# Kernel optimization log

Measured on AMD Instinct MI355X. Metric: run time of the kernel, lower is better.

Reference implementation:

```python
import jax, jax.numpy as jnp
import numpy as np

N = 50000
NEG_SLOPE = 0.2


def add_self_loops(edge_index, n):
    loop = jnp.arange(n, dtype=edge_index.dtype)
    return jnp.concatenate([edge_index, jnp.stack([loop, loop])], axis=1)


def gatv2_conv(x, edge_index, Wl, bl, Wr, br, att, bias):
    """PyG GATv2Conv (share_weights=False, concat=True, add_self_loops applied by caller).
    x: [N, Fin]; edge_index: [2, E] with row0=src(j), row1=dst(i); att: [H, D].
    Returns (out [N, H*D], alpha [E, H])."""
    src, dst = edge_index[0], edge_index[1]
    H, D = att.shape
    n = x.shape[0]
    xl = (x @ Wl + bl).reshape(n, H, D)   # source-side transform
    xr = (x @ Wr + br).reshape(n, H, D)   # target-side transform
    e = jax.nn.leaky_relu(xl[src] + xr[dst], NEG_SLOPE)        # [E, H, D]
    logit = jnp.einsum('ehd,hd->eh', e, att)                    # [E, H]
    # segment softmax over edges grouped by target node
    lmax = jax.ops.segment_max(logit, dst, num_segments=n)      # [N, H]
    ex = jnp.exp(logit - lmax[dst])
    denom = jax.ops.segment_sum(ex, dst, num_segments=n)
    alpha = ex / denom[dst]                                     # [E, H]
    out = jax.ops.segment_sum(alpha[:, :, None] * xl[src], dst, num_segments=n)  # [N, H, D]
    return out.reshape(n, H * D) + bias, alpha


def setup_inputs() -> dict:
    key = jax.random.key(0)
    ks = jax.random.split(key, 16)
    E = 400000
    x = jax.random.normal(ks[0], (N, 23), dtype=jnp.float32)
    edge_index = jax.random.randint(ks[1], (2, E), 0, N, dtype=jnp.int64)
    H1, D1 = 8, 64
    F1 = H1 * D1  # 512
    s = 0.1
    return {
        'x': x,
        'edge_index': edge_index,
        'Wl1': jax.random.normal(ks[2], (23, F1), dtype=jnp.float32) * s,
        'bl1': jnp.zeros((F1,), jnp.float32),
        'Wr1': jax.random.normal(ks[3], (23, F1), dtype=jnp.float32) * s,
        'br1': jnp.zeros((F1,), jnp.float32),
        'att1': jax.random.normal(ks[4], (H1, D1), dtype=jnp.float32) * s,
        'bias1': jnp.zeros((F1,), jnp.float32),
        'Wl2': jax.random.normal(ks[5], (F1, 1), dtype=jnp.float32) * s,
        'bl2': jnp.zeros((1,), jnp.float32),
        'Wr2': jax.random.normal(ks[6], (F1, 1), dtype=jnp.float32) * s,
        'br2': jnp.zeros((1,), jnp.float32),
        'att2': jax.random.normal(ks[7], (1, 1), dtype=jnp.float32) * s,
        'bias2': jnp.zeros((1,), jnp.float32),
    }


def reference(x, edge_index, Wl1, bl1, Wr1, br1, att1, bias1,
              Wl2, bl2, Wr2, br2, att2, bias2):
    ei = add_self_loops(edge_index, N)
    h, _ = gatv2_conv(x, ei, Wl1, bl1, Wr1, br1, att1, bias1)
    h = jax.nn.relu(h)
    h, alpha = gatv2_conv(h, ei, Wl2, bl2, Wr2, br2, att2, bias2)
    return h, alpha
```

## Files before the change

### kernel.cpp

```cpp
#include <hip/hip_runtime.h>
#include <math.h>

#define NN 50000
#define E0 400000
#define EE 450000
#define FF 512
#define G1 2048
#define NPB 25
#define EPB 220
#define WAVES_TOTAL (G1 * 4)
#define MAXD 64
#define LOG2E 1.44269504f

typedef _Float16 h2 __attribute__((ext_vector_type(2)));

__device__ __forceinline__ h2 uas_h2(unsigned u) { union { unsigned u; h2 h; } c; c.u = u; return c.h; }
__device__ __forceinline__ unsigned h2as_u(h2 h) { union { unsigned u; h2 h; } c; c.h = h; return c.u; }
__device__ __forceinline__ unsigned packh(float a, float b) {
    h2 hh = { (_Float16)a, (_Float16)b };
    return h2as_u(hh);
}
__device__ __forceinline__ float leaky(float v) { return fmaxf(v, 0.2f * v); }

__global__ __launch_bounds__(256) void k_predeg(
    const float* __restrict__ x,
    const float* __restrict__ Wl1, const float* __restrict__ bl1,
    const float* __restrict__ Wr1, const float* __restrict__ br1,
    const int* __restrict__ ei,
    unsigned* __restrict__ xlh, unsigned* __restrict__ xrh,
    int* __restrict__ cnt, int* __restrict__ src_sl, int* __restrict__ eid_sl)
{
    __shared__ unsigned sxh[NPB * 12];
    int b = blockIdx.x, t = threadIdx.x;

    {
        int e0 = b * EPB;
        int e1 = e0 + EPB; if (e1 > EE) e1 = EE;
        for (int e = e0 + t; e < e1; e += 256) {
            int src, dst;
            if (e < E0) { src = ei[e]; dst = ei[E0 + e]; }
            else        { src = e - E0; dst = src; }
            int p = atomicAdd(&cnt[dst], 1);
            if (p < MAXD) {
                src_sl[(size_t)dst * MAXD + p] = src;
                eid_sl[(size_t)dst * MAXD + p] = e;
            }
        }
    }

    int i0 = b * NPB;
    int i1 = i0 + NPB; if (i1 > NN) i1 = NN;
    int nnod = i1 - i0;
    for (int k = t; k < nnod * 12; k += 256) {
        int n = k / 12, j = k - n * 12;
        const float* row = x + (size_t)(i0 + n) * 23;
        float f0 = row[2 * j];
        float f1 = (2 * j + 1 < 23) ? row[2 * j + 1] : 0.f;
        sxh[n * 12 + j] = packh(f0, f1);
    }

    int c0 = 2 * t, c1 = 2 * t + 1;
    h2 wl0[12], wl1[12], wr0[12], wr1[12];
#pragma unroll
    for (int j = 0; j < 12; j++) {
        int r0 = 2 * j, r1 = 2 * j + 1;
        float a, b2;
        a = Wl1[r0 * FF + c0]; b2 = (r1 < 23) ? Wl1[r1 * FF + c0] : 0.f;
        wl0[j] = (h2){ (_Float16)a, (_Float16)b2 };
        a = Wl1[r0 * FF + c1]; b2 = (r1 < 23) ? Wl1[r1 * FF + c1] : 0.f;
        wl1[j] = (h2){ (_Float16)a, (_Float16)b2 };
        a = Wr1[r0 * FF + c0]; b2 = (r1 < 23) ? Wr1[r1 * FF + c0] : 0.f;
        wr0[j] = (h2){ (_Float16)a, (_Float16)b2 };
        a = Wr1[r0 * FF + c1]; b2 = (r1 < 23) ? Wr1[r1 * FF + c1] : 0.f;
        wr1[j] = (h2){ (_Float16)a, (_Float16)b2 };
    }
    float bl0 = bl1[c0], bl1s = bl1[c1];
    float br0 = br1[c0], br1s = br1[c1];
    __syncthreads();

    const uint4* S = (const uint4*)sxh;
    for (int n = 0; n < nnod; n++) {
        uint4 xa = S[n * 3 + 0];
        uint4 xb = S[n * 3 + 1];
        uint4 xc = S[n * 3 + 2];
        h2 xv[12] = { uas_h2(xa.x), uas_h2(xa.y), uas_h2(xa.z), uas_h2(xa.w),
                      uas_h2(xb.x), uas_h2(xb.y), uas_h2(xb.z), uas_h2(xb.w),
                      uas_h2(xc.x), uas_h2(xc.y), uas_h2(xc.z), uas_h2(xc.w) };
        float al0 = bl0, al1 = bl1s, ar0 = br0, ar1 = br1s;
#pragma unroll
        for (int j = 0; j < 12; j++) {
            al0 = __builtin_amdgcn_fdot2(wl0[j], xv[j], al0, false);
            al1 = __builtin_amdgcn_fdot2(wl1[j], xv[j], al1, false);
            ar0 = __builtin_amdgcn_fdot2(wr0[j], xv[j], ar0, false);
            ar1 = __builtin_amdgcn_fdot2(wr1[j], xv[j], ar1, false);
        }
        xlh[(size_t)(i0 + n) * 256 + t] = packh(al0, al1);
        xrh[(size_t)(i0 + n) * 256 + t] = packh(ar0, ar1);
    }
}

__global__ __launch_bounds__(256) void k_layer1(
    const uint4* __restrict__ xlh, const uint4* __restrict__ xrh,
    const float* __restrict__ att, const float* __restrict__ bias1,
    const float* __restrict__ Wl2, const float* __restrict__ bl2,
    const float* __restrict__ Wr2, const float* __restrict__ br2,
    const int* __restrict__ cnt, const int* __restrict__ src_sl,
    float* __restrict__ xl2, float* __restrict__ xr2)
{
    int t = threadIdx.x;
    int l = t & 63;
    int wid = blockIdx.x * 4 + (t >> 6);

    float4 atA = ((const float4*)att)[2 * l];
    float4 atB = ((const float4*)att)[2 * l + 1];
    h2 a6_0 = { (_Float16)(0.6f * LOG2E * atA.x), (_Float16)(0.6f * LOG2E * atA.y) };
    h2 a6_1 = { (_Float16)(0.6f * LOG2E * atA.z), (_Float16)(0.6f * LOG2E * atA.w) };
    h2 a6_2 = { (_Float16)(0.6f * LOG2E * atB.x), (_Float16)(0.6f * LOG2E * atB.y) };
    h2 a6_3 = { (_Float16)(0.6f * LOG2E * atB.z), (_Float16)(0.6f * LOG2E * atB.w) };
    h2 a4_0 = { (_Float16)(0.4f * LOG2E * atA.x), (_Float16)(0.4f * LOG2E * atA.y) };
    h2 a4_1 = { (_Float16)(0.4f * LOG2E * atA.z), (_Float16)(0.4f * LOG2E * atA.w) };
    h2 a4_2 = { (_Float16)(0.4f * LOG2E * atB.x), (_Float16)(0.4f * LOG2E * atB.y) };
    h2 a4_3 = { (_Float16)(0.4f * LOG2E * atB.z), (_Float16)(0.4f * LOG2E * atB.w) };
    float bl2v = bl2[0], br2v = br2[0];

    for (int i = wid; i < NN; i += WAVES_TOTAL) {
        uint4 xq = xrh[(size_t)i * 64 + l];
        h2 q0 = uas_h2(xq.x), q1 = uas_h2(xq.y), q2 = uas_h2(xq.z), q3 = uas_h2(xq.w);

        float s = 0.f;
        h2 A0 = { 0, 0 }, A1 = { 0, 0 }, A2 = { 0, 0 }, A3 = { 0, 0 };

        int dg = cnt[i]; if (dg > MAXD) dg = MAXD;
        int myj = (l < dg) ? src_sl[(size_t)i * MAXD + l] : 0;

        int j0 = __builtin_amdgcn_readlane(myj, 0);
        uint4 r0 = xlh[(size_t)j0 * 64 + l];
        uint4 r1 = r0;
        if (dg > 1) r1 = xlh[(size_t)__builtin_amdgcn_readlane(myj, 1) * 64 + l];

        for (int p = 0; p < dg; p++) {
            uint4 rn = r0;
            if (p + 2 < dg)
                rn = xlh[(size_t)__builtin_amdgcn_readlane(myj, p + 2) * 64 + l];

            h2 p0 = uas_h2(r0.x), p1 = uas_h2(r0.y), p2 = uas_h2(r0.z), p3 = uas_h2(r0.w);
            h2 t0 = p0 + q0, t1 = p1 + q1, t2 = p2 + q2, t3 = p3 + q3;
            h2 b0 = uas_h2(h2as_u(t0) & 0x7fff7fffu);
            h2 b1 = uas_h2(h2as_u(t1) & 0x7fff7fffu);
            h2 b2 = uas_h2(h2as_u(t2) & 0x7fff7fffu);
            h2 b3 = uas_h2(h2as_u(t3) & 0x7fff7fffu);
            float part = 0.f;
            part = __builtin_amdgcn_fdot2(a6_0, t0, part, false);
            part = __builtin_amdgcn_fdot2(a4_0, b0, part, false);
            part = __builtin_amdgcn_fdot2(a6_1, t1, part, false);
            part = __builtin_amdgcn_fdot2(a4_1, b1, part, false);
            part = __builtin_amdgcn_fdot2(a6_2, t2, part, false);
            part = __builtin_amdgcn_fdot2(a4_2, b2, part, false);
            part = __builtin_amdgcn_fdot2(a6_3, t3, part, false);
            part = __builtin_amdgcn_fdot2(a4_3, b3, part, false);
            part += __shfl_xor(part, 1, 64);
            part += __shfl_xor(part, 2, 64);
            part += __shfl_xor(part, 4, 64);
            float wv = exp2f(part);
            s += wv;
            _Float16 wh = (_Float16)wv;
            h2 w2 = { wh, wh };
            A0 += w2 * p0;
            A1 += w2 * p1;
            A2 += w2 * p2;
            A3 += w2 * p3;
            r0 = r1; r1 = rn;
        }

        float inv = 1.f / s;
        float4 bA = ((const float4*)bias1)[2 * l];
        float4 bB = ((const float4*)bias1)[2 * l + 1];
        float h0 = fmaxf(fmaf((float)A0[0], inv, bA.x), 0.f);
        float h1 = fmaxf(fmaf((float)A0[1], inv, bA.y), 0.f);
        float h2v = fmaxf(fmaf((float)A1[0], inv, bA.z), 0.f);
        float h3 = fmaxf(fmaf((float)A1[1], inv, bA.w), 0.f);
        float h4 = fmaxf(fmaf((float)A2[0], inv, bB.x), 0.f);
        float h5 = fmaxf(fmaf((float)A2[1], inv, bB.y), 0.f);
        float h6 = fmaxf(fmaf((float)A3[0], inv, bB.z), 0.f);
        float h7 = fmaxf(fmaf((float)A3[1], inv, bB.w), 0.f);

        float4 wlA = ((const float4*)Wl2)[2 * l];
        float4 wlB = ((const float4*)Wl2)[2 * l + 1];
        float4 wrA = ((const float4*)Wr2)[2 * l];
        float4 wrB = ((const float4*)Wr2)[2 * l + 1];
        float pl = h0 * wlA.x + h1 * wlA.y + h2v * wlA.z + h3 * wlA.w
                 + h4 * wlB.x + h5 * wlB.y + h6 * wlB.z + h7 * wlB.w;
        float pr = h0 * wrA.x + h1 * wrA.y + h2v * wrA.z + h3 * wrA.w
                 + h4 * wrB.x + h5 * wrB.y + h6 * wrB.z + h7 * wrB.w;
#pragma unroll
        for (int o = 32; o > 0; o >>= 1) {
            pl += __shfl_xor(pl, o, 64);
            pr += __shfl_xor(pr, o, 64);
        }
        if (l == 0) {
            xl2[i] = pl + bl2v;
            xr2[i] = pr + br2v;
        }
    }
}

__global__ void k_layer2(const float* __restrict__ xl2, const float* __restrict__ xr2,
                         const float* __restrict__ att2, const float* __restrict__ bias2,
                         const int* __restrict__ cnt, const int* __restrict__ src_sl,
                         const int* __restrict__ eid_sl, float* __restrict__ out)
{
    int i = blockIdx.x * blockDim.x + threadIdx.x;
    if (i >= NN) return;
    int dg = cnt[i]; if (dg > MAXD) dg = MAXD;
    const int* sp = src_sl + (size_t)i * MAXD;
    const int* ep = eid_sl + (size_t)i * MAXD;
    float xri = xr2[i];
    float a2l = att2[0] * LOG2E;
    float s = 0.f, num = 0.f;
    for (int p = 0; p < dg; p++) {
        float v = xl2[sp[p]];
        float w = exp2f(leaky(v + xri) * a2l);
        s += w;
        num = fmaf(w, v, num);
    }
    out[i] = num / s + bias2[0];
    float inv = 1.f / s;
    for (int p = 0; p < dg; p++) {
        float v = xl2[sp[p]];
        float w = exp2f(leaky(v + xri) * a2l);
        out[NN + ep[p]] = w * inv;
    }
}

extern "C" void kernel_launch(void* const* d_in, const int* in_sizes, int n_in,
                              void* d_out, int out_size, void* d_ws, size_t ws_size,
                              hipStream_t stream)
{
    const float* x     = (const float*)d_in[0];
    const int*   ei    = (const int*)d_in[1];
    const float* Wl1   = (const float*)d_in[2];
    const float* bl1   = (const float*)d_in[3];
    const float* Wr1   = (const float*)d_in[4];
    const float* br1   = (const float*)d_in[5];
    const float* att1  = (const float*)d_in[6];
    const float* bias1 = (const float*)d_in[7];
    const float* Wl2   = (const float*)d_in[8];
    const float* bl2   = (const float*)d_in[9];
    const float* Wr2   = (const float*)d_in[10];
    const float* br2   = (const float*)d_in[11];
    const float* att2  = (const float*)d_in[12];
    const float* bias2 = (const float*)d_in[13];
    float* out = (float*)d_out;

    char* ws = (char*)d_ws;
    unsigned* xlh  = (unsigned*)ws; ws += (size_t)NN * 256 * 4;
    unsigned* xrh  = (unsigned*)ws; ws += (size_t)NN * 256 * 4;
    float* xl2     = (float*)ws;    ws += (size_t)NN * 4;
    float* xr2     = (float*)ws;    ws += (size_t)NN * 4;
    int* cnt       = (int*)ws;      ws += (size_t)NN * 4;
    int* src_sl    = (int*)ws;      ws += (size_t)NN * MAXD * 4;
    int* eid_sl    = (int*)ws;      ws += (size_t)NN * MAXD * 4;

    hipMemsetAsync(cnt, 0, (size_t)NN * 4, stream);

    k_predeg<<<G1, 256, 0, stream>>>(x, Wl1, bl1, Wr1, br1, ei, xlh, xrh,
                                     cnt, src_sl, eid_sl);
    k_layer1<<<G1, 256, 0, stream>>>((const uint4*)xlh, (const uint4*)xrh,
                                     att1, bias1, Wl2, bl2, Wr2, br2,
                                     cnt, src_sl, xl2, xr2);
    k_layer2<<<(NN + 255) / 256, 256, 0, stream>>>(xl2, xr2, att2, bias2,
                                                   cnt, src_sl, eid_sl, out);
}
```

Measured before the change: 238.7 us.

## Fuse three kernels into one persistent kernel with software grid barriers

Merges the degree/projection, layer-1 aggregation and layer-2 kernels into a single persistent kernel of 1024 blocks. The stages are separated by atomic-counter grid barriers instead of kernel launch boundaries. Per-block work sizes are doubled to match the halved grid, and the barrier counters are zeroed by the existing memset. This removes two launch gaps but adds spin-wait barrier cost. The barriers assume all 1024 blocks are resident at once, which is not guaranteed by a plain launch, and a block that is not resident would deadlock.

Measured after the change: 737.5 us. 3.09x slower.

```diff
diff --git a/kernel.cpp b/kernel.cpp
--- a/kernel.cpp
+++ b/kernel.cpp
@@ -5,10 +5,10 @@
 #define E0 400000
 #define EE 450000
 #define FF 512
-#define G1 2048
-#define NPB 25
-#define EPB 220
-#define WAVES_TOTAL (G1 * 4)
+#define GRID 1024
+#define NPB 49
+#define EPB 440
+#define L1W (GRID * 4)
 #define MAXD 64
 #define LOG2E 1.44269504f
 
@@ -22,13 +22,32 @@
 }
 __device__ __forceinline__ float leaky(float v) { return fmaxf(v, 0.2f * v); }
 
-__global__ __launch_bounds__(256) void k_predeg(
-    const float* __restrict__ x,
+__device__ __forceinline__ void gridbar(int* bar, int* rel, int t)
+{
+    __threadfence();
+    __syncthreads();
+    if (t == 0) {
+        int v = atomicAdd(bar, 1);
+        if (v == GRID - 1) atomicExch(rel, 1);
+        else while (atomicAdd(rel, 0) == 0) __builtin_amdgcn_s_sleep(16);
+    }
+    __syncthreads();
+    __threadfence();
+}
+
+__global__ __launch_bounds__(256, 4) void k_mega(
+    const float* __restrict__ x, const int* __restrict__ ei,
     const float* __restrict__ Wl1, const float* __restrict__ bl1,
     const float* __restrict__ Wr1, const float* __restrict__ br1,
-    const int* __restrict__ ei,
+    const float* __restrict__ att1, const float* __restrict__ bias1,
+    const float* __restrict__ Wl2, const float* __restrict__ bl2,
+    const float* __restrict__ Wr2, const float* __restrict__ br2,
+    const float* __restrict__ att2, const float* __restrict__ bias2,
+    float* __restrict__ out,
     unsigned* __restrict__ xlh, unsigned* __restrict__ xrh,
-    int* __restrict__ cnt, int* __restrict__ src_sl, int* __restrict__ eid_sl)
+    float* __restrict__ xl2, float* __restrict__ xr2,
+    int* __restrict__ cnt, int* __restrict__ bar,
+    int* __restrict__ src_sl, int* __restrict__ eid_sl)
 {
     __shared__ unsigned sxh[NPB * 12];
     int b = blockIdx.x, t = threadIdx.x;
@@ -46,189 +65,182 @@
                 eid_sl[(size_t)dst * MAXD + p] = e;
             }
         }
-    }
-
-    int i0 = b * NPB;
-    int i1 = i0 + NPB; if (i1 > NN) i1 = NN;
-    int nnod = i1 - i0;
-    for (int k = t; k < nnod * 12; k += 256) {
-        int n = k / 12, j = k - n * 12;
-        const float* row = x + (size_t)(i0 + n) * 23;
-        float f0 = row[2 * j];
-        float f1 = (2 * j + 1 < 23) ? row[2 * j + 1] : 0.f;
-        sxh[n * 12 + j] = packh(f0, f1);
-    }
-
-    int c0 = 2 * t, c1 = 2 * t + 1;
-    h2 wl0[12], wl1[12], wr0[12], wr1[12];
-#pragma unroll
-    for (int j = 0; j < 12; j++) {
-        int r0 = 2 * j, r1 = 2 * j + 1;
-        float a, b2;
-        a = Wl1[r0 * FF + c0]; b2 = (r1 < 23) ? Wl1[r1 * FF + c0] : 0.f;
-        wl0[j] = (h2){ (_Float16)a, (_Float16)b2 };
-        a = Wl1[r0 * FF + c1]; b2 = (r1 < 23) ? Wl1[r1 * FF + c1] : 0.f;
-        wl1[j] = (h2){ (_Float16)a, (_Float16)b2 };
-        a = Wr1[r0 * FF + c0]; b2 = (r1 < 23) ? Wr1[r1 * FF + c0] : 0.f;
-        wr0[j] = (h2){ (_Float16)a, (_Float16)b2 };
-        a = Wr1[r0 * FF + c1]; b2 = (r1 < 23) ? Wr1[r1 * FF + c1] : 0.f;
-        wr1[j] = (h2){ (_Float16)a, (_Float16)b2 };
-    }
-    float bl0 = bl1[c0], bl1s = bl1[c1];
-    float br0 = br1[c0], br1s = br1[c1];
-    __syncthreads();
-
-    const uint4* S = (const uint4*)sxh;
-    for (int n = 0; n < nnod; n++) {
-        uint4 xa = S[n * 3 + 0];
-        uint4 xb = S[n * 3 + 1];
-        uint4 xc = S[n * 3 + 2];
-        h2 xv[12] = { uas_h2(xa.x), uas_h2(xa.y), uas_h2(xa.z), uas_h2(xa.w),
-                      uas_h2(xb.x), uas_h2(xb.y), uas_h2(xb.z), uas_h2(xb.w),
-                      uas_h2(xc.x), uas_h2(xc.y), uas_h2(xc.z), uas_h2(xc.w) };
-        float al0 = bl0, al1 = bl1s, ar0 = br0, ar1 = br1s;
+
+        int i0 = b * NPB;
+        int i1 = i0 + NPB; if (i1 > NN) i1 = NN; if (i1 < i0) i1 = i0;
+        int nnod = i1 - i0;
+        for (int k = t; k < nnod * 12; k += 256) {
+            int n = k / 12, j = k - n * 12;
+            const float* row = x + (size_t)(i0 + n) * 23;
+            float f0 = row[2 * j];
+            float f1 = (2 * j + 1 < 23) ? row[2 * j + 1] : 0.f;
+            sxh[n * 12 + j] = packh(f0, f1);
+        }
+
+        int c0 = 2 * t, c1 = 2 * t + 1;
+        h2 wl0[12], wl1[12], wr0[12], wr1[12];
 #pragma unroll
         for (int j = 0; j < 12; j++) {
-            al0 = __builtin_amdgcn_fdot2(wl0[j], xv[j], al0, false);
-            al1 = __builtin_amdgcn_fdot2(wl1[j], xv[j], al1, false);
-            ar0 = __builtin_amdgcn_fdot2(wr0[j], xv[j], ar0, false);
-            ar1 = __builtin_amdgcn_fdot2(wr1[j], xv[j], ar1, false);
-        }
-        xlh[(size_t)(i0 + n) * 256 + t] = packh(al0, al1);
-        xrh[(size_t)(i0 + n) * 256 + t] = packh(ar0, ar1);
-    }
-}
-
-__global__ __launch_bounds__(256) void k_layer1(
-    const uint4* __restrict__ xlh, const uint4* __restrict__ xrh,
-    const float* __restrict__ att, const float* __restrict__ bias1,
-    const float* __restrict__ Wl2, const float* __restrict__ bl2,
-    const float* __restrict__ Wr2, const float* __restrict__ br2,
-    const int* __restrict__ cnt, const int* __restrict__ src_sl,
-    float* __restrict__ xl2, float* __restrict__ xr2)
-{
-    int t = threadIdx.x;
-    int l = t & 63;
-    int wid = blockIdx.x * 4 + (t >> 6);
-
-    float4 atA = ((const float4*)att)[2 * l];
-    float4 atB = ((const float4*)att)[2 * l + 1];
-    h2 a6_0 = { (_Float16)(0.6f * LOG2E * atA.x), (_Float16)(0.6f * LOG2E * atA.y) };
-    h2 a6_1 = { (_Float16)(0.6f * LOG2E * atA.z), (_Float16)(0.6f * LOG2E * atA.w) };
-    h2 a6_2 = { (_Float16)(0.6f * LOG2E * atB.x), (_Float16)(0.6f * LOG2E * atB.y) };
-    h2 a6_3 = { (_Float16)(0.6f * LOG2E * atB.z), (_Float16)(0.6f * LOG2E * atB.w) };
-    h2 a4_0 = { (_Float16)(0.4f * LOG2E * atA.x), (_Float16)(0.4f * LOG2E * atA.y) };
-    h2 a4_1 = { (_Float16)(0.4f * LOG2E * atA.z), (_Float16)(0.4f * LOG2E * atA.w) };
-    h2 a4_2 = { (_Float16)(0.4f * LOG2E * atB.x), (_Float16)(0.4f * LOG2E * atB.y) };
-    h2 a4_3 = { (_Float16)(0.4f * LOG2E * atB.z), (_Float16)(0.4f * LOG2E * atB.w) };
-    float bl2v = bl2[0], br2v = br2[0];
-
-    for (int i = wid; i < NN; i += WAVES_TOTAL) {
-        uint4 xq = xrh[(size_t)i * 64 + l];
-        h2 q0 = uas_h2(xq.x), q1 = uas_h2(xq.y), q2 = uas_h2(xq.z), q3 = uas_h2(xq.w);
-
-        float s = 0.f;
-        h2 A0 = { 0, 0 }, A1 = { 0, 0 }, A2 = { 0, 0 }, A3 = { 0, 0 };
-
-        int dg = cnt[i]; if (dg > MAXD) dg = MAXD;
-        int myj = (l < dg) ? src_sl[(size_t)i * MAXD + l] : 0;
-
-        int j0 = __builtin_amdgcn_readlane(myj, 0);
-        uint4 r0 = xlh[(size_t)j0 * 64 + l];
-        uint4 r1 = r0;
-        if (dg > 1) r1 = xlh[(size_t)__builtin_amdgcn_readlane(myj, 1) * 64 + l];
-
-        for (int p = 0; p < dg; p++) {
-            uint4 rn = r0;
-            if (p + 2 < dg)
-                rn = xlh[(size_t)__builtin_amdgcn_readlane(myj, p + 2) * 64 + l];
-
-            h2 p0 = uas_h2(r0.x), p1 = uas_h2(r0.y), p2 = uas_h2(r0.z), p3 = uas_h2(r0.w);
-            h2 t0 = p0 + q0, t1 = p1 + q1, t2 = p2 + q2, t3 = p3 + q3;
-            h2 b0 = uas_h2(h2as_u(t0) & 0x7fff7fffu);
-            h2 b1 = uas_h2(h2as_u(t1) & 0x7fff7fffu);
-            h2 b2 = uas_h2(h2as_u(t2) & 0x7fff7fffu);
-            h2 b3 = uas_h2(h2as_u(t3) & 0x7fff7fffu);
-            float part = 0.f;
-            part = __builtin_amdgcn_fdot2(a6_0, t0, part, false);
-            part = __builtin_amdgcn_fdot2(a4_0, b0, part, false);
-            part = __builtin_amdgcn_fdot2(a6_1, t1, part, false);
-            part = __builtin_amdgcn_fdot2(a4_1, b1, part, false);
-            part = __builtin_amdgcn_fdot2(a6_2, t2, part, false);
-            part = __builtin_amdgcn_fdot2(a4_2, b2, part, false);
-            part = __builtin_amdgcn_fdot2(a6_3, t3, part, false);
-            part = __builtin_amdgcn_fdot2(a4_3, b3, part, false);
-            part += __shfl_xor(part, 1, 64);
-            part += __shfl_xor(part, 2, 64);
-            part += __shfl_xor(part, 4, 64);
-            float wv = exp2f(part);
-            s += wv;
-            _Float16 wh = (_Float16)wv;
-            h2 w2 = { wh, wh };
-            A0 += w2 * p0;
-            A1 += w2 * p1;
-            A2 += w2 * p2;
-            A3 += w2 * p3;
-            r0 = r1; r1 = rn;
-        }
-
-        float inv = 1.f / s;
-        float4 bA = ((const float4*)bias1)[2 * l];
-        float4 bB = ((const float4*)bias1)[2 * l + 1];
-        float h0 = fmaxf(fmaf((float)A0[0], inv, bA.x), 0.f);
-        float h1 = fmaxf(fmaf((float)A0[1], inv, bA.y), 0.f);
-        float h2v = fmaxf(fmaf((float)A1[0], inv, bA.z), 0.f);
-        float h3 = fmaxf(fmaf((float)A1[1], inv, bA.w), 0.f);
-        float h4 = fmaxf(fmaf((float)A2[0], inv, bB.x), 0.f);
-        float h5 = fmaxf(fmaf((float)A2[1], inv, bB.y), 0.f);
-        float h6 = fmaxf(fmaf((float)A3[0], inv, bB.z), 0.f);
-        float h7 = fmaxf(fmaf((float)A3[1], inv, bB.w), 0.f);
-
-        float4 wlA = ((const float4*)Wl2)[2 * l];
-        float4 wlB = ((const float4*)Wl2)[2 * l + 1];
-        float4 wrA = ((const float4*)Wr2)[2 * l];
-        float4 wrB = ((const float4*)Wr2)[2 * l + 1];
-        float pl = h0 * wlA.x + h1 * wlA.y + h2v * wlA.z + h3 * wlA.w
-                 + h4 * wlB.x + h5 * wlB.y + h6 * wlB.z + h7 * wlB.w;
-        float pr = h0 * wrA.x + h1 * wrA.y + h2v * wrA.z + h3 * wrA.w
-                 + h4 * wrB.x + h5 * wrB.y + h6 * wrB.z + h7 * wrB.w;
+            int r0 = 2 * j, r1 = 2 * j + 1;
+            float a, b2;
+            a = Wl1[r0 * FF + c0]; b2 = (r1 < 23) ? Wl1[r1 * FF + c0] : 0.f;
+            wl0[j] = (h2){ (_Float16)a, (_Float16)b2 };
+            a = Wl1[r0 * FF + c1]; b2 = (r1 < 23) ? Wl1[r1 * FF + c1] : 0.f;
+            wl1[j] = (h2){ (_Float16)a, (_Float16)b2 };
+            a = Wr1[r0 * FF + c0]; b2 = (r1 < 23) ? Wr1[r1 * FF + c0] : 0.f;
+            wr0[j] = (h2){ (_Float16)a, (_Float16)b2 };
+            a = Wr1[r0 * FF + c1]; b2 = (r1 < 23) ? Wr1[r1 * FF + c1] : 0.f;
+            wr1[j] = (h2){ (_Float16)a, (_Float16)b2 };
+        }
+        float bl0 = bl1[c0], bl1s = bl1[c1];
+        float br0 = br1[c0], br1s = br1[c1];
+        __syncthreads();
+
+        const uint4* S = (const uint4*)sxh;
+        for (int n = 0; n < nnod; n++) {
+            uint4 xa = S[n * 3 + 0];
+            uint4 xb = S[n * 3 + 1];
+            uint4 xc = S[n * 3 + 2];
+            h2 xv[12] = { uas_h2(xa.x), uas_h2(xa.y), uas_h2(xa.z), uas_h2(xa.w),
+                          uas_h2(xb.x), uas_h2(xb.y), uas_h2(xb.z), uas_h2(xb.w),
+                          uas_h2(xc.x), uas_h2(xc.y), uas_h2(xc.z), uas_h2(xc.w) };
+            float al0 = bl0, al1 = bl1s, ar0 = br0, ar1 = br1s;
 #pragma unroll
-        for (int o = 32; o > 0; o >>= 1) {
-            pl += __shfl_xor(pl, o, 64);
-            pr += __shfl_xor(pr, o, 64);
-        }
-        if (l == 0) {
-            xl2[i] = pl + bl2v;
-            xr2[i] = pr + br2v;
-        }
-    }
-}
-
-__global__ void k_layer2(const float* __restrict__ xl2, const float* __restrict__ xr2,
-                         const float* __restrict__ att2, const float* __restrict__ bias2,
-                         const int* __restrict__ cnt, const int* __restrict__ src_sl,
-                         const int* __restrict__ eid_sl, float* __restrict__ out)
-{
-    int i = blockIdx.x * blockDim.x + threadIdx.x;
-    if (i >= NN) return;
-    int dg = cnt[i]; if (dg > MAXD) dg = MAXD;
-    const int* sp = src_sl + (size_t)i * MAXD;
-    const int* ep = eid_sl + (size_t)i * MAXD;
-    float xri = xr2[i];
-    float a2l = att2[0] * LOG2E;
-    float s = 0.f, num = 0.f;
-    for (int p = 0; p < dg; p++) {
-        float v = xl2[sp[p]];
-        float w = exp2f(leaky(v + xri) * a2l);
-        s += w;
-        num = fmaf(w, v, num);
-    }
-    out[i] = num / s + bias2[0];
-    float inv = 1.f / s;
-    for (int p = 0; p < dg; p++) {
-        float v = xl2[sp[p]];
-        float w = exp2f(leaky(v + xri) * a2l);
-        out[NN + ep[p]] = w * inv;
+            for (int j = 0; j < 12; j++) {
+                al0 = __builtin_amdgcn_fdot2(wl0[j], xv[j], al0, false);
+                al1 = __builtin_amdgcn_fdot2(wl1[j], xv[j], al1, false);
+                ar0 = __builtin_amdgcn_fdot2(wr0[j], xv[j], ar0, false);
+                ar1 = __builtin_amdgcn_fdot2(wr1[j], xv[j], ar1, false);
+            }
+            xlh[(size_t)(i0 + n) * 256 + t] = packh(al0, al1);
+            xrh[(size_t)(i0 + n) * 256 + t] = packh(ar0, ar1);
+        }
+    }
+    gridbar(&bar[0], &bar[1], t);
+
+    {
+        const uint4* xl4 = (const uint4*)xlh;
+        const uint4* xr4 = (const uint4*)xrh;
+        int l = t & 63;
+        int wid = b * 4 + (t >> 6);
+
+        float4 atA = ((const float4*)att1)[2 * l];
+        float4 atB = ((const float4*)att1)[2 * l + 1];
+        h2 a6_0 = { (_Float16)(0.6f * LOG2E * atA.x), (_Float16)(0.6f * LOG2E * atA.y) };
+        h2 a6_1 = { (_Float16)(0.6f * LOG2E * atA.z), (_Float16)(0.6f * LOG2E * atA.w) };
+        h2 a6_2 = { (_Float16)(0.6f * LOG2E * atB.x), (_Float16)(0.6f * LOG2E * atB.y) };
+        h2 a6_3 = { (_Float16)(0.6f * LOG2E * atB.z), (_Float16)(0.6f * LOG2E * atB.w) };
+        h2 a4_0 = { (_Float16)(0.4f * LOG2E * atA.x), (_Float16)(0.4f * LOG2E * atA.y) };
+        h2 a4_1 = { (_Float16)(0.4f * LOG2E * atA.z), (_Float16)(0.4f * LOG2E * atA.w) };
+        h2 a4_2 = { (_Float16)(0.4f * LOG2E * atB.x), (_Float16)(0.4f * LOG2E * atB.y) };
+        h2 a4_3 = { (_Float16)(0.4f * LOG2E * atB.z), (_Float16)(0.4f * LOG2E * atB.w) };
+        float bl2v = bl2[0], br2v = br2[0];
+
+        for (int i = wid; i < NN; i += L1W) {
+            uint4 xq = xr4[(size_t)i * 64 + l];
+            h2 q0 = uas_h2(xq.x), q1 = uas_h2(xq.y), q2 = uas_h2(xq.z), q3 = uas_h2(xq.w);
+
+            float s = 0.f;
+            h2 A0 = { 0, 0 }, A1 = { 0, 0 }, A2 = { 0, 0 }, A3 = { 0, 0 };
+
+            int dg = cnt[i]; if (dg > MAXD) dg = MAXD;
+            int myj = (l < dg) ? src_sl[(size_t)i * MAXD + l] : 0;
+
+            int j0 = __builtin_amdgcn_readlane(myj, 0);
+            uint4 r0 = xl4[(size_t)j0 * 64 + l];
+            uint4 r1 = r0;
+            if (dg > 1) r1 = xl4[(size_t)__builtin_amdgcn_readlane(myj, 1) * 64 + l];
+
+            for (int p = 0; p < dg; p++) {
+                uint4 rn = r0;
+                if (p + 2 < dg)
+                    rn = xl4[(size_t)__builtin_amdgcn_readlane(myj, p + 2) * 64 + l];
+
+                h2 p0 = uas_h2(r0.x), p1 = uas_h2(r0.y), p2 = uas_h2(r0.z), p3 = uas_h2(r0.w);
+                h2 t0 = p0 + q0, t1 = p1 + q1, t2 = p2 + q2, t3 = p3 + q3;
+                h2 b0 = uas_h2(h2as_u(t0) & 0x7fff7fffu);
+                h2 b1 = uas_h2(h2as_u(t1) & 0x7fff7fffu);
+                h2 b2 = uas_h2(h2as_u(t2) & 0x7fff7fffu);
+                h2 b3 = uas_h2(h2as_u(t3) & 0x7fff7fffu);
+                float part = 0.f;
+                part = __builtin_amdgcn_fdot2(a6_0, t0, part, false);
+                part = __builtin_amdgcn_fdot2(a4_0, b0, part, false);
+                part = __builtin_amdgcn_fdot2(a6_1, t1, part, false);
+                part = __builtin_amdgcn_fdot2(a4_1, b1, part, false);
+                part = __builtin_amdgcn_fdot2(a6_2, t2, part, false);
+                part = __builtin_amdgcn_fdot2(a4_2, b2, part, false);
+                part = __builtin_amdgcn_fdot2(a6_3, t3, part, false);
+                part = __builtin_amdgcn_fdot2(a4_3, b3, part, false);
+                part += __shfl_xor(part, 1, 64);
+                part += __shfl_xor(part, 2, 64);
+                part += __shfl_xor(part, 4, 64);
+                float wv = exp2f(part);
+                s += wv;
+                _Float16 wh = (_Float16)wv;
+                h2 w2 = { wh, wh };
+                A0 += w2 * p0;
+                A1 += w2 * p1;
+                A2 += w2 * p2;
+                A3 += w2 * p3;
+                r0 = r1; r1 = rn;
+            }
+
+            float inv = 1.f / s;
+            float4 bA = ((const float4*)bias1)[2 * l];
+            float4 bB = ((const float4*)bias1)[2 * l + 1];
+            float h0 = fmaxf(fmaf((float)A0[0], inv, bA.x), 0.f);
+            float h1 = fmaxf(fmaf((float)A0[1], inv, bA.y), 0.f);
+            float h2v = fmaxf(fmaf((float)A1[0], inv, bA.z), 0.f);
+            float h3 = fmaxf(fmaf((float)A1[1], inv, bA.w), 0.f);
+            float h4 = fmaxf(fmaf((float)A2[0], inv, bB.x), 0.f);
+            float h5 = fmaxf(fmaf((float)A2[1], inv, bB.y), 0.f);
+            float h6 = fmaxf(fmaf((float)A3[0], inv, bB.z), 0.f);
+            float h7 = fmaxf(fmaf((float)A3[1], inv, bB.w), 0.f);
+
+            float4 wlA = ((const float4*)Wl2)[2 * l];
+            float4 wlB = ((const float4*)Wl2)[2 * l + 1];
+            float4 wrA = ((const float4*)Wr2)[2 * l];
+            float4 wrB = ((const float4*)Wr2)[2 * l + 1];
+            float pl = h0 * wlA.x + h1 * wlA.y + h2v * wlA.z + h3 * wlA.w
+                     + h4 * wlB.x + h5 * wlB.y + h6 * wlB.z + h7 * wlB.w;
+            float pr = h0 * wrA.x + h1 * wrA.y + h2v * wrA.z + h3 * wrA.w
+                     + h4 * wrB.x + h5 * wrB.y + h6 * wrB.z + h7 * wrB.w;
+#pragma unroll
+            for (int o = 32; o > 0; o >>= 1) {
+                pl += __shfl_xor(pl, o, 64);
+                pr += __shfl_xor(pr, o, 64);
+            }
+            if (l == 0) {
+                xl2[i] = pl + bl2v;
+                xr2[i] = pr + br2v;
+            }
+        }
+    }
+    gridbar(&bar[2], &bar[3], t);
+
+    {
+        int i = b * 256 + t;
+        if (i < NN) {
+            int dg = cnt[i]; if (dg > MAXD) dg = MAXD;
+            const int* sp = src_sl + (size_t)i * MAXD;
+            const int* ep = eid_sl + (size_t)i * MAXD;
+            float xri = xr2[i];
+            float a2l = att2[0] * LOG2E;
+            float s = 0.f, num = 0.f;
+            for (int p = 0; p < dg; p++) {
+                float v = xl2[sp[p]];
+                float w = exp2f(leaky(v + xri) * a2l);
+                s += w;
+                num = fmaf(w, v, num);
+            }
+            out[i] = num / s + bias2[0];
+            float inv = 1.f / s;
+            for (int p = 0; p < dg; p++) {
+                float v = xl2[sp[p]];
+                float w = exp2f(leaky(v + xri) * a2l);
+                out[NN + ep[p]] = w * inv;
+            }
+        }
     }
 }
 
@@ -258,16 +270,18 @@
     float* xl2     = (float*)ws;    ws += (size_t)NN * 4;
     float* xr2     = (float*)ws;    ws += (size_t)NN * 4;
     int* cnt       = (int*)ws;      ws += (size_t)NN * 4;
+    int* bar       = (int*)ws;      ws += (size_t)16 * 4;
     int* src_sl    = (int*)ws;      ws += (size_t)NN * MAXD * 4;
     int* eid_sl    = (int*)ws;      ws += (size_t)NN * MAXD * 4;
 
-    hipMemsetAsync(cnt, 0, (size_t)NN * 4, stream);
-
-    k_predeg<<<G1, 256, 0, stream>>>(x, Wl1, bl1, Wr1, br1, ei, xlh, xrh,
-                                     cnt, src_sl, eid_sl);
-    k_layer1<<<G1, 256, 0, stream>>>((const uint4*)xlh, (const uint4*)xrh,
-                                     att1, bias1, Wl2, bl2, Wr2, br2,
-                                     cnt, src_sl, xl2, xr2);
-    k_layer2<<<(NN + 255) / 256, 256, 0, stream>>>(xl2, xr2, att2, bias2,
-                                                   cnt, src_sl, eid_sl, out);
-}
+    hipMemsetAsync(cnt, 0, (size_t)(NN + 16) * 4, stream);
+
+    void* kargs[] = {
+        (void*)&x, (void*)&ei, (void*)&Wl1, (void*)&bl1, (void*)&Wr1, (void*)&br1,
+        (void*)&att1, (void*)&bias1, (void*)&Wl2, (void*)&bl2, (void*)&Wr2, (void*)&br2,
+        (void*)&att2, (void*)&bias2, (void*)&out,
+        (void*)&xlh, (void*)&xrh, (void*)&xl2, (void*)&xr2,
+        (void*)&cnt, (void*)&bar, (void*)&src_sl, (void*)&eid_sl
+    };
+    hipLaunchKernel((const void*)k_mega, dim3(GRID), dim3(256), kargs, 0, stream);
+}
```

## Write layer-2 attention coefficients in edge order via separate per-edge kernel

Applied to the files above, without the earlier changes.

Drops the per-node edge-id slot table and its scattered stores during degree bucketing. Layer 2 is split into a per-node kernel that computes the output and stores the inverse softmax denominator, and a per-edge kernel that recomputes each coefficient and writes alpha contiguously. This trades an extra launch and recomputation of the edge logit for coalesced writes and less memory traffic.

New measurement: 228.0 us. 4.5% less time.

```diff
diff --git a/kernel.cpp b/kernel.cpp
--- a/kernel.cpp
+++ b/kernel.cpp
@@ -28,7 +28,7 @@
     const float* __restrict__ Wr1, const float* __restrict__ br1,
     const int* __restrict__ ei,
     unsigned* __restrict__ xlh, unsigned* __restrict__ xrh,
-    int* __restrict__ cnt, int* __restrict__ src_sl, int* __restrict__ eid_sl)
+    int* __restrict__ cnt, int* __restrict__ src_sl)
 {
     __shared__ unsigned sxh[NPB * 12];
     int b = blockIdx.x, t = threadIdx.x;
@@ -41,10 +41,7 @@
             if (e < E0) { src = ei[e]; dst = ei[E0 + e]; }
             else        { src = e - E0; dst = src; }
             int p = atomicAdd(&cnt[dst], 1);
-            if (p < MAXD) {
-                src_sl[(size_t)dst * MAXD + p] = src;
-                eid_sl[(size_t)dst * MAXD + p] = e;
-            }
+            if (p < MAXD) src_sl[(size_t)dst * MAXD + p] = src;
         }
     }
 
@@ -204,16 +201,15 @@
     }
 }
 
-__global__ void k_layer2(const float* __restrict__ xl2, const float* __restrict__ xr2,
-                         const float* __restrict__ att2, const float* __restrict__ bias2,
-                         const int* __restrict__ cnt, const int* __restrict__ src_sl,
-                         const int* __restrict__ eid_sl, float* __restrict__ out)
+__global__ void k_layer2a(const float* __restrict__ xl2, const float* __restrict__ xr2,
+                          const float* __restrict__ att2, const float* __restrict__ bias2,
+                          const int* __restrict__ cnt, const int* __restrict__ src_sl,
+                          float* __restrict__ out, float* __restrict__ invs)
 {
     int i = blockIdx.x * blockDim.x + threadIdx.x;
     if (i >= NN) return;
     int dg = cnt[i]; if (dg > MAXD) dg = MAXD;
     const int* sp = src_sl + (size_t)i * MAXD;
-    const int* ep = eid_sl + (size_t)i * MAXD;
     float xri = xr2[i];
     float a2l = att2[0] * LOG2E;
     float s = 0.f, num = 0.f;
@@ -224,12 +220,21 @@
         num = fmaf(w, v, num);
     }
     out[i] = num / s + bias2[0];
-    float inv = 1.f / s;
-    for (int p = 0; p < dg; p++) {
-        float v = xl2[sp[p]];
-        float w = exp2f(leaky(v + xri) * a2l);
-        out[NN + ep[p]] = w * inv;
-    }
+    invs[i] = 1.f / s;
+}
+
+__global__ void k_layer2b(const float* __restrict__ xl2, const float* __restrict__ xr2,
+                          const float* __restrict__ att2, const int* __restrict__ ei,
+                          const float* __restrict__ invs, float* __restrict__ out)
+{
+    int e = blockIdx.x * blockDim.x + threadIdx.x;
+    if (e >= EE) return;
+    int src, dst;
+    if (e < E0) { src = ei[e]; dst = ei[E0 + e]; }
+    else        { src = e - E0; dst = src; }
+    float a2l = att2[0] * LOG2E;
+    float lg = leaky(xl2[src] + xr2[dst]) * a2l;
+    out[NN + e] = exp2f(lg) * invs[dst];
 }
 
 extern "C" void kernel_launch(void* const* d_in, const int* in_sizes, int n_in,
@@ -257,17 +262,18 @@
     unsigned* xrh  = (unsigned*)ws; ws += (size_t)NN * 256 * 4;
     float* xl2     = (float*)ws;    ws += (size_t)NN * 4;
     float* xr2     = (float*)ws;    ws += (size_t)NN * 4;
+    float* invs    = (float*)ws;    ws += (size_t)NN * 4;
     int* cnt       = (int*)ws;      ws += (size_t)NN * 4;
     int* src_sl    = (int*)ws;      ws += (size_t)NN * MAXD * 4;
-    int* eid_sl    = (int*)ws;      ws += (size_t)NN * MAXD * 4;
 
     hipMemsetAsync(cnt, 0, (size_t)NN * 4, stream);
 
     k_predeg<<<G1, 256, 0, stream>>>(x, Wl1, bl1, Wr1, br1, ei, xlh, xrh,
-                                     cnt, src_sl, eid_sl);
+                                     cnt, src_sl);
     k_layer1<<<G1, 256, 0, stream>>>((const uint4*)xlh, (const uint4*)xrh,
                                      att1, bias1, Wl2, bl2, Wr2, br2,
                                      cnt, src_sl, xl2, xr2);
-    k_layer2<<<(NN + 255) / 256, 256, 0, stream>>>(xl2, xr2, att2, bias2,
-                                                   cnt, src_sl, eid_sl, out);
-}
+    k_layer2a<<<(NN + 255) / 256, 256, 0, stream>>>(xl2, xr2, att2, bias2,
+                                                    cnt, src_sl, out, invs);
+    k_layer2b<<<(EE + 255) / 256, 256, 0, stream>>>(xl2, xr2, att2, ei, invs, out);
+}
```
